# Kernel optimization log

Measured on AMD Instinct MI355X. Metric: run time of the kernel, lower is better.

## Reference

```python
import jax, jax.numpy as jnp
import numpy as np
from jax import lax

B, D, E, H, W = 256, 64, 16, 64, 64
PROJ, FC, NA = 512, 1024, 2

def _conv(x, w, pad):
    # x: [N,C,H,W], w: [O,I,kh,kw]
    return lax.conv_general_dilated(x, w, (1, 1), [(pad, pad), (pad, pad)],
                                    dimension_numbers=('NCHW', 'OIHW', 'NCHW'))

def _maxpool2(x):
    return lax.reduce_window(x, -jnp.inf, lax.max, (1, 1, 2, 2), (1, 1, 2, 2), 'VALID')

def _sample_conv(x, w, b):
    # per-sample conv with its own gathered expert weights: x [D,h,w], w [D,D,3,3]
    y = lax.conv_general_dilated(x[None], w, (1, 1), [(1, 1), (1, 1)],
                                 dimension_numbers=('NCHW', 'OIHW', 'NCHW'))[0]
    return y + b[:, None, None]

_expert_conv = jax.vmap(_sample_conv)  # batch of samples, each with its own kernel

def setup_inputs() -> dict:
    key = jax.random.key(0)
    ks = jax.random.split(key, 12)
    s = 0.05
    return {
        'image': jax.random.normal(ks[0], (B, 3, H, W), jnp.float32),
        'question': jax.random.randint(ks[1], (B, 8), 0, E),
        'stem_w0': jax.random.normal(ks[2], (D, 3, 3, 3), jnp.float32) * s,
        'stem_b0': jnp.zeros((D,), jnp.float32),
        'stem_w': jax.random.normal(ks[3], (3, D, D, 3, 3), jnp.float32) * s,
        'stem_b': jnp.zeros((3, D), jnp.float32),
        'exp_w1': jax.random.normal(ks[4], (E, D, D, 3, 3), jnp.float32) * s,
        'exp_b1': jnp.zeros((E, D), jnp.float32),
        'exp_w2': jax.random.normal(ks[5], (E, D, D, 3, 3), jnp.float32) * s,
        'exp_b2': jnp.zeros((E, D), jnp.float32),
        'proj_w': jax.random.normal(ks[6], (PROJ, D, 1, 1), jnp.float32) * s,
        'proj_b': jnp.zeros((PROJ,), jnp.float32),
        'fc1_w': jax.random.normal(ks[7], (FC, PROJ * 8 * 8), jnp.float32) * 0.01,
        'fc1_b': jnp.zeros((FC,), jnp.float32),
        'fc2_w': jax.random.normal(ks[8], (NA, FC), jnp.float32) * 0.01,
        'fc2_b': jnp.zeros((NA,), jnp.float32),
    }

def reference(image, question, stem_w0, stem_b0, stem_w, stem_b,
              exp_w1, exp_b1, exp_w2, exp_b2,
              proj_w, proj_b, fc1_w, fc1_b, fc2_w, fc2_b):
    # --- stem: 4 conv3x3 + ReLU, maxpool after layers 0 and 2 (64->32->16) ---
    h = jax.nn.relu(_conv(image, stem_w0, 1) + stem_b0[None, :, None, None])
    h = _maxpool2(h)
    h = jax.nn.relu(_conv(h, stem_w[0], 1) + stem_b[0][None, :, None, None])
    h = jax.nn.relu(_conv(h, stem_w[1], 1) + stem_b[1][None, :, None, None])
    h = _maxpool2(h)
    h = jax.nn.relu(_conv(h, stem_w[2], 1) + stem_b[2][None, :, None, None])
    # --- chain1 routing: cols (lhs=4, rel=5, rhs=7) each pick a ResidualBlock expert ---
    for col in (4, 5, 7):
        idx = question[:, col]                       # [B] expert ids
        w1, b1 = exp_w1[idx], exp_b1[idx]            # gather per-sample kernels
        w2, b2 = exp_w2[idx], exp_b2[idx]
        mid = jax.nn.relu(_expert_conv(h, w1, b1))   # conv1 + ReLU
        out = _expert_conv(mid, w2, b2)              # conv2 (no BN)
        h = jax.nn.relu(h + out)                     # residual + ReLU
    # --- classifier: 1x1 proj + ReLU, maxpool2, flatten, fc, fc ---
    c = jax.nn.relu(_conv(h, proj_w, 0) + proj_b[None, :, None, None])  # [B,512,16,16]
    c = _maxpool2(c)                                                     # [B,512,8,8]
    c = c.reshape(c.shape[0], -1)                                        # [B,32768]
    c = jax.nn.relu(c @ fc1_w.T + fc1_b)
    return c @ fc2_w.T + fc2_b                                           # [B,2]
```

## Files before the change

### kernel.cpp

```cpp
#include <hip/hip_runtime.h>
#include <cstddef>


typedef _Float16 half8 __attribute__((ext_vector_type(8)));
typedef _Float16 half4_t __attribute__((ext_vector_type(4)));
typedef float f32x4 __attribute__((ext_vector_type(4)));

#define LO_SCALE 2048.0f
#define LO_INV (1.0f / 2048.0f)

__global__ void transw_k(const float* __restrict__ src, float* __restrict__ dst,
                         int O, int I, int K, int total) {
    int id = blockIdx.x * 256 + threadIdx.x;
    if (id >= total) return;
    int OIK = O * I * K;
    int n = id / OIK, rem = id % OIK;
    int o = rem / (I * K), r2 = rem % (I * K);
    int i = r2 / K, k = r2 % K;
    dst[(size_t)n * OIK + (i * K + k) * O + o] = src[id];
}

__global__ void wxform_k(const float* __restrict__ src, _Float16* __restrict__ dst,
                         int nlayers) {
    int id = blockIdx.x * 256 + threadIdx.x;
    if (id >= nlayers * 36864) return;
    int layer = id / 36864, idx = id % 36864;
    int j = idx & 7, l = (idx >> 3) & 63, nt = (idx >> 9) & 3;
    int icc = (idx >> 11) & 1, tap = idx >> 12;
    int kl = (l >> 4) * 8 + j, ic = icc * 32 + kl, oc = nt * 16 + (l & 15);
    float v = src[(size_t)layer * 36864 + (oc * 64 + ic) * 9 + tap];
    _Float16 hi = (_Float16)v;
    _Float16 lo = (_Float16)((v - (float)hi) * LO_SCALE);
    dst[(size_t)layer * 73728 + idx] = hi;
    dst[(size_t)layer * 73728 + 36864 + idx] = lo;
}

__global__ void pwxform_k(const float* __restrict__ src, _Float16* __restrict__ dst) {
    int id = blockIdx.x * 256 + threadIdx.x;
    if (id >= 32768) return;
    int j = id & 7, l = (id >> 3) & 63, icc = (id >> 9) & 1, nt = id >> 10;
    int kl = (l >> 4) * 8 + j, ic = icc * 32 + kl, oc = nt * 16 + (l & 15);
    float v = src[oc * 64 + ic];
    _Float16 hi = (_Float16)v;
    _Float16 lo = (_Float16)((v - (float)hi) * LO_SCALE);
    dst[id] = hi;
    dst[32768 + id] = lo;
}

__global__ __launch_bounds__(256)
void conv1_k(const float* __restrict__ img, const float* __restrict__ w0t,
             const float* __restrict__ b0, float* __restrict__ out) {
    int b = blockIdx.x, tile = blockIdx.y, ocg = blockIdx.z;
    int typ = (tile >> 1) * 16, txp = (tile & 1) * 16;
    int cy0 = typ * 2, cx0 = txp * 2;
    __shared__ float lds[3][34][34];
    const float* imb = img + (size_t)b * 3 * 64 * 64;
    for (int i = threadIdx.x; i < 3 * 34 * 34; i += 256) {
        int c = i / 1156, rem = i % 1156, r = rem / 34, cc = rem % 34;
        int gy = cy0 - 1 + r, gx = cx0 - 1 + cc;
        float v = 0.f;
        if (gy >= 0 && gy < 64 && gx >= 0 && gx < 64) v = imb[(c * 64 + gy) * 64 + gx];
        lds[c][r][cc] = v;
    }
    __syncthreads();
    int pyl = threadIdx.x >> 4, pxl = threadIdx.x & 15;
    float win[3][4][4];
#pragma unroll
    for (int c = 0; c < 3; ++c)
#pragma unroll
        for (int wy = 0; wy < 4; ++wy)
#pragma unroll
            for (int wx = 0; wx < 4; ++wx)
                win[c][wy][wx] = lds[c][2 * pyl + wy][2 * pxl + wx];
    int py = typ + pyl, px = txp + pxl;
    float* op = &out[(((size_t)b * 32 + py) * 32 + px) * 64];
#pragma unroll
    for (int q = 0; q < 4; ++q) {
        int ocq = ocg * 4 + q;
        float acc[4][4] = {};
#pragma unroll
        for (int c = 0; c < 3; ++c)
#pragma unroll
            for (int ky = 0; ky < 3; ++ky)
#pragma unroll
                for (int kx = 0; kx < 3; ++kx) {
                    float4 w = *(const float4*)&w0t[(c * 9 + ky * 3 + kx) * 64 + ocq * 4];
                    float wv4[4] = {w.x, w.y, w.z, w.w};
#pragma unroll
                    for (int p2 = 0; p2 < 4; ++p2) {
                        float iv = win[c][(p2 >> 1) + ky][(p2 & 1) + kx];
#pragma unroll
                        for (int o = 0; o < 4; ++o)
                            acc[p2][o] = fmaf(iv, wv4[o], acc[p2][o]);
                    }
                }
        float4 res;
        float* rp = (float*)&res;
#pragma unroll
        for (int o = 0; o < 4; ++o) {
            float bvv = b0[ocq * 4 + o];
            float m = fmaxf(fmaxf(acc[0][o], acc[1][o]), fmaxf(acc[2][o], acc[3][o]));
            rp[o] = fmaxf(m + bvv, 0.f);
        }
        *(float4*)&op[ocq * 4] = res;
    }
}

template <int S, bool POOL, bool RES>
__global__ __launch_bounds__(256, 2)
void convm_k(const float* __restrict__ in, float* __restrict__ out,
             const _Float16* __restrict__ wf, const float* __restrict__ bias,
             const float* __restrict__ res, const int* __restrict__ question,
             int qcol) {
    int b = blockIdx.x, t = blockIdx.y;
    constexpr int NTX = S / 16;
    int ty0 = (t / NTX) * 8, tx0 = (t % NTX) * 16;

    __shared__ __align__(16) _Float16 lds[2 * 7200];

    int tid = threadIdx.x, lane = tid & 63, wv = tid >> 6;
    const _Float16* wb = wf;
    const float* bb = bias;
    if (question) {
        int idx = question[b * 8 + qcol];
        wb += (size_t)idx * 73728;
        bb += idx * 64;
    }
    float bv[4];
#pragma unroll
    for (int nt = 0; nt < 4; ++nt) bv[nt] = bb[nt * 16 + (lane & 15)];

    f32x4 acc1[2][4] = {};
    f32x4 acc2[2][4] = {};

    int am = lane & 15;
    int k0 = (lane >> 4) * 8;

    for (int icc = 0; icc < 2; ++icc) {
        __syncthreads();
        for (int i = tid; i < 1440; i += 256) {
            int pix = i >> 3, j4 = i & 7;
            int hy = pix / 18, hx = pix % 18;
            int gy = ty0 + hy - 1, gx = tx0 + hx - 1;
            float4 v = {0.f, 0.f, 0.f, 0.f};
            if (gy >= 0 && gy < S && gx >= 0 && gx < S)
                v = *(const float4*)&in[(((size_t)b * S + gy) * S + gx) * 64 + icc * 32 + j4 * 4];
            _Float16 h0 = (_Float16)v.x, h1 = (_Float16)v.y;
            _Float16 h2 = (_Float16)v.z, h3 = (_Float16)v.w;
            half4_t hh = {h0, h1, h2, h3};
            half4_t ll = {(_Float16)((v.x - (float)h0) * LO_SCALE),
                          (_Float16)((v.y - (float)h1) * LO_SCALE),
                          (_Float16)((v.z - (float)h2) * LO_SCALE),
                          (_Float16)((v.w - (float)h3) * LO_SCALE)};
            *(half4_t*)&lds[pix * 40 + j4 * 4] = hh;
            *(half4_t*)&lds[7200 + pix * 40 + j4 * 4] = ll;
        }
        __syncthreads();

#pragma unroll
        for (int ky = 0; ky < 3; ++ky)
#pragma unroll
            for (int kx = 0; kx < 3; ++kx) {
                int tap = ky * 3 + kx;
                const _Float16* wp = wb + (tap * 2 + icc) * 2048 + lane * 8;
                half8 bhi[4], blo[4];
#pragma unroll
                for (int nt = 0; nt < 4; ++nt) {
                    bhi[nt] = *(const half8*)(wp + nt * 512);
                    blo[nt] = *(const half8*)(wp + nt * 512 + 36864);
                }
#pragma unroll
                for (int mt = 0; mt < 2; ++mt) {
                    int MT = wv * 2 + mt;
                    int Q = MT * 4 + (am >> 2), s = am & 3;
                    int py = (Q >> 3) * 2 + (s >> 1), px = (Q & 7) * 2 + (s & 1);
                    const _Float16* ap = &lds[((py + ky) * 18 + (px + kx)) * 40 + k0];
                    half8 ahi = *(const half8*)ap;
                    half8 alo = *(const half8*)(ap + 7200);
#pragma unroll
                    for (int nt = 0; nt < 4; ++nt) {
                        acc1[mt][nt] = __builtin_amdgcn_mfma_f32_16x16x32_f16(
                            ahi, bhi[nt], acc1[mt][nt], 0, 0, 0);
                        acc2[mt][nt] = __builtin_amdgcn_mfma_f32_16x16x32_f16(
                            ahi, blo[nt], acc2[mt][nt], 0, 0, 0);
                        acc2[mt][nt] = __builtin_amdgcn_mfma_f32_16x16x32_f16(
                            alo, bhi[nt], acc2[mt][nt], 0, 0, 0);
                    }
                }
            }
    }

    int cn = lane & 15, rq = lane >> 4;
#pragma unroll
    for (int mt = 0; mt < 2; ++mt) {
        int MT = wv * 2 + mt;
        int Q = MT * 4 + rq;
        int qy = Q >> 3, qx = Q & 7;
#pragma unroll
        for (int nt = 0; nt < 4; ++nt) {
            int oc = nt * 16 + cn;
            float vals[4];
#pragma unroll
            for (int r = 0; r < 4; ++r)
                vals[r] = acc1[mt][nt][r] + acc2[mt][nt][r] * LO_INV + bv[nt];
            if (POOL) {
                float m = fmaxf(fmaxf(vals[0], vals[1]), fmaxf(vals[2], vals[3]));
                m = fmaxf(m, 0.f);
                int opy = (ty0 >> 1) + qy, opx = (tx0 >> 1) + qx;
                out[(((size_t)b * (S / 2) + opy) * (S / 2) + opx) * 64 + oc] = m;
            } else {
#pragma unroll
                for (int r = 0; r < 4; ++r) {
                    int py = qy * 2 + (r >> 1), px = qx * 2 + (r & 1);
                    size_t o = (((size_t)b * S + (ty0 + py)) * S + (tx0 + px)) * 64 + oc;
                    float v = vals[r];
                    if (RES) v += res[o];
                    out[o] = fmaxf(v, 0.f);
                }
            }
        }
    }
}

__global__ __launch_bounds__(256)
void projm_k(const float* __restrict__ in ,
             const _Float16* __restrict__ pw, const float* __restrict__ bias,
             _Float16* __restrict__ outh ) {
    int b = blockIdx.x;
    __shared__ float lt[64 * 65];
    int tid = threadIdx.x, lane = tid & 63, wv = tid >> 6;
    int row = lane & 15, cseg = lane >> 4;

    half8 ah[4][2], al[4][2];
#pragma unroll
    for (int mt = 0; mt < 4; ++mt) {
        int MT = wv * 4 + mt;
        int Q = MT * 4 + (row >> 2), s = row & 3;
        int y = (Q >> 3) * 2 + (s >> 1), x = (Q & 7) * 2 + (s & 1);
        const float* ip = in + ((size_t)b * 256 + y * 16 + x) * 64 + cseg * 8;
#pragma unroll
        for (int icc = 0; icc < 2; ++icc) {
            float4 v0 = *(const float4*)(ip + icc * 32);
            float4 v1 = *(const float4*)(ip + icc * 32 + 4);
            _Float16 h0 = (_Float16)v0.x, h1 = (_Float16)v0.y;
            _Float16 h2 = (_Float16)v0.z, h3 = (_Float16)v0.w;
            _Float16 h4 = (_Float16)v1.x, h5 = (_Float16)v1.y;
            _Float16 h6 = (_Float16)v1.z, h7 = (_Float16)v1.w;
            ah[mt][icc] = (half8){h0, h1, h2, h3, h4, h5, h6, h7};
            al[mt][icc] = (half8){(_Float16)((v0.x - (float)h0) * LO_SCALE),
                                  (_Float16)((v0.y - (float)h1) * LO_SCALE),
                                  (_Float16)((v0.z - (float)h2) * LO_SCALE),
                                  (_Float16)((v0.w - (float)h3) * LO_SCALE),
                                  (_Float16)((v1.x - (float)h4) * LO_SCALE),
                                  (_Float16)((v1.y - (float)h5) * LO_SCALE),
                                  (_Float16)((v1.z - (float)h6) * LO_SCALE),
                                  (_Float16)((v1.w - (float)h7) * LO_SCALE)};
        }
    }

    for (int ogl = 0; ogl < 4; ++ogl) {
        int og = blockIdx.y * 4 + ogl;
        half8 bh[4][2], bl[4][2];
#pragma unroll
        for (int ntl = 0; ntl < 4; ++ntl)
#pragma unroll
            for (int icc = 0; icc < 2; ++icc) {
                int nt = og * 4 + ntl;
                const _Float16* wp = pw + ((nt * 2 + icc) * 64 + lane) * 8;
                bh[ntl][icc] = *(const half8*)wp;
                bl[ntl][icc] = *(const half8*)(wp + 32768);
            }
        f32x4 a1[4][4] = {};
        f32x4 a2[4][4] = {};
#pragma unroll
        for (int icc = 0; icc < 2; ++icc)
#pragma unroll
            for (int mt = 0; mt < 4; ++mt)
#pragma unroll
                for (int ntl = 0; ntl < 4; ++ntl) {
                    a1[mt][ntl] = __builtin_amdgcn_mfma_f32_16x16x32_f16(
                        ah[mt][icc], bh[ntl][icc], a1[mt][ntl], 0, 0, 0);
                    a2[mt][ntl] = __builtin_amdgcn_mfma_f32_16x16x32_f16(
                        ah[mt][icc], bl[ntl][icc], a2[mt][ntl], 0, 0, 0);
                    a2[mt][ntl] = __builtin_amdgcn_mfma_f32_16x16x32_f16(
                        al[mt][icc], bh[ntl][icc], a2[mt][ntl], 0, 0, 0);
                }
        if (ogl) __syncthreads();
#pragma unroll
        for (int mt = 0; mt < 4; ++mt) {
            int Qg = (wv * 4 + mt) * 4 + (lane >> 4);
#pragma unroll
            for (int ntl = 0; ntl < 4; ++ntl) {
                float bvv = bias[og * 64 + ntl * 16 + (lane & 15)];
                float v0 = a1[mt][ntl][0] + a2[mt][ntl][0] * LO_INV + bvv;
                float v1 = a1[mt][ntl][1] + a2[mt][ntl][1] * LO_INV + bvv;
                float v2 = a1[mt][ntl][2] + a2[mt][ntl][2] * LO_INV + bvv;
                float v3 = a1[mt][ntl][3] + a2[mt][ntl][3] * LO_INV + bvv;
                float m = fmaxf(fmaxf(fmaxf(v0, v1), fmaxf(v2, v3)), 0.f);
                lt[(ntl * 16 + (lane & 15)) * 65 + Qg] = m;
            }
        }
        __syncthreads();
#pragma unroll
        for (int r = 0; r < 16; ++r) {
            int f = r * 256 + tid;
            int ol = f >> 6, q = f & 63;
            float v = lt[ol * 65 + q];
            _Float16 h = (_Float16)v;
            _Float16 l = (_Float16)((v - (float)h) * LO_SCALE);
            size_t o = (size_t)b * 32768 + og * 4096 + ol * 64 + q;
            outh[o] = h;
            outh[8388608 + o] = l;
        }
    }
}

__global__ __launch_bounds__(256)
void fc1m_k(const _Float16* __restrict__ Ahl ,
            const float* __restrict__ W,
            float* __restrict__ partial ) {
    int bid = blockIdx.x;
    int lid = (bid & 7) * 64 + (bid >> 3);
    int mt = lid & 1, nt = (lid >> 1) & 7, ks = lid >> 4;
    int m0 = mt * 128, n0 = nt * 128;
    const _Float16* Ab = Ahl + (size_t)m0 * 32768 + ks * 1024;
    const float* Wb = W + (size_t)n0 * 32768 + ks * 1024;

    __shared__ __align__(16) _Float16 lds[20480];
    _Float16* sa = lds;
    _Float16* sb = lds + 10240;

    int tid = threadIdx.x, lane = tid & 63, wv = tid >> 6;
    int wm = (wv & 1) * 64, wn = (wv >> 1) * 64;

    f32x4 acc1[4][4] = {};
    f32x4 acc2[4][4] = {};

    int arow[2], ak8[2];
#pragma unroll
    for (int p = 0; p < 2; ++p) {
        int idx = p * 256 + tid;
        arow[p] = idx >> 2;
        ak8[p] = (idx & 3) * 8;
    }
    int wrow[4], wc4[4];
#pragma unroll
    for (int p = 0; p < 4; ++p) {
        int idx = p * 256 + tid;
        wrow[p] = idx >> 3;
        wc4[p] = (idx & 7) << 2;
    }

    half8 pa_h[2], pa_l[2];
    float4 rw[4];
#pragma unroll
    for (int p = 0; p < 2; ++p) {
        pa_h[p] = *(const half8*)&Ab[(size_t)arow[p] * 32768 + ak8[p]];
        pa_l[p] = *(const half8*)&Ab[8388608 + (size_t)arow[p] * 32768 + ak8[p]];
    }
#pragma unroll
    for (int p = 0; p < 4; ++p)
        rw[p] = *(const float4*)&Wb[(size_t)wrow[p] * 32768 + wc4[p]];

    for (int kt = 0; kt < 32; ++kt) {
#pragma unroll
        for (int p = 0; p < 2; ++p) {
            *(half8*)&sa[arow[p] * 40 + ak8[p]] = pa_h[p];
            *(half8*)&sa[5120 + arow[p] * 40 + ak8[p]] = pa_l[p];
        }
#pragma unroll
        for (int p = 0; p < 4; ++p) {
            float4 u = rw[p];
            _Float16 g0 = (_Float16)u.x, g1 = (_Float16)u.y;
            _Float16 g2 = (_Float16)u.z, g3 = (_Float16)u.w;
            half4_t gh = {g0, g1, g2, g3};
            half4_t gl = {(_Float16)((u.x - (float)g0) * LO_SCALE),
                          (_Float16)((u.y - (float)g1) * LO_SCALE),
                          (_Float16)((u.z - (float)g2) * LO_SCALE),
                          (_Float16)((u.w - (float)g3) * LO_SCALE)};
            *(half4_t*)&sb[wrow[p] * 40 + wc4[p]] = gh;
            *(half4_t*)&sb[5120 + wrow[p] * 40 + wc4[p]] = gl;
        }
        __syncthreads();
        if (kt < 31) {
            int kb = (kt + 1) * 32;
#pragma unroll
            for (int p = 0; p < 2; ++p) {
                pa_h[p] = *(const half8*)&Ab[(size_t)arow[p] * 32768 + kb + ak8[p]];
                pa_l[p] = *(const half8*)&Ab[8388608 + (size_t)arow[p] * 32768 + kb + ak8[p]];
            }
#pragma unroll
            for (int p = 0; p < 4; ++p)
                rw[p] = *(const float4*)&Wb[(size_t)wrow[p] * 32768 + kb + wc4[p]];
        }
        int koff = (lane >> 4) * 8;
        int fr = lane & 15;
        half8 bh[4], bl[4];
#pragma unroll
        for (int nf = 0; nf < 4; ++nf) {
            int r = wn + nf * 16 + fr;
            bh[nf] = *(const half8*)&sb[r * 40 + koff];
            bl[nf] = *(const half8*)&sb[5120 + r * 40 + koff];
        }
#pragma unroll
        for (int mf = 0; mf < 4; ++mf) {
            int r = wm + mf * 16 + fr;
            half8 ah = *(const half8*)&sa[r * 40 + koff];
            half8 al = *(const half8*)&sa[5120 + r * 40 + koff];
#pragma unroll
            for (int nf = 0; nf < 4; ++nf) {
                acc1[mf][nf] = __builtin_amdgcn_mfma_f32_16x16x32_f16(
                    ah, bh[nf], acc1[mf][nf], 0, 0, 0);
                acc2[mf][nf] = __builtin_amdgcn_mfma_f32_16x16x32_f16(
                    ah, bl[nf], acc2[mf][nf], 0, 0, 0);
                acc2[mf][nf] = __builtin_amdgcn_mfma_f32_16x16x32_f16(
                    al, bh[nf], acc2[mf][nf], 0, 0, 0);
            }
        }
        __syncthreads();
    }

    int rq = lane >> 4, cn = lane & 15;
    float* pb = partial + (size_t)ks * 262144;
#pragma unroll
    for (int mf = 0; mf < 4; ++mf)
#pragma unroll
        for (int nf = 0; nf < 4; ++nf) {
            int n = n0 + wn + nf * 16 + cn;
#pragma unroll
            for (int r = 0; r < 4; ++r) {
                int m = m0 + wm + mf * 16 + rq * 4 + r;
                pb[(size_t)m * 1024 + n] = acc1[mf][nf][r] + acc2[mf][nf][r] * LO_INV;
            }
        }
}

__global__ __launch_bounds__(256)
void fc1red_k(const float* __restrict__ partial, const float* __restrict__ b1,
              float* __restrict__ fc1o_t ) {
    int m = blockIdx.x;
    int n0 = threadIdx.x * 4;
    float4 s = {0.f, 0.f, 0.f, 0.f};
    for (int ks = 0; ks < 32; ++ks) {
        float4 v = *(const float4*)&partial[((size_t)ks * 256 + m) * 1024 + n0];
        s.x += v.x; s.y += v.y; s.z += v.z; s.w += v.w;
    }
    fc1o_t[(size_t)(n0 + 0) * 256 + m] = fmaxf(s.x + b1[n0 + 0], 0.f);
    fc1o_t[(size_t)(n0 + 1) * 256 + m] = fmaxf(s.y + b1[n0 + 1], 0.f);
    fc1o_t[(size_t)(n0 + 2) * 256 + m] = fmaxf(s.z + b1[n0 + 2], 0.f);
    fc1o_t[(size_t)(n0 + 3) * 256 + m] = fmaxf(s.w + b1[n0 + 3], 0.f);
}

__global__ __launch_bounds__(256)
void fc2a_k(const float* __restrict__ a_t, const float* __restrict__ W2,
            float* __restrict__ p2) {
    int n2 = blockIdx.x, ks = blockIdx.y;
    int m = threadIdx.x;
    float acc = 0.f;
    for (int k = ks * 256; k < ks * 256 + 256; ++k)
        acc = fmaf(a_t[(size_t)k * 256 + m], W2[n2 * 1024 + k], acc);
    p2[((size_t)n2 * 4 + ks) * 256 + m] = acc;
}

__global__ __launch_bounds__(512)
void fc2b_k(const float* __restrict__ p2, const float* __restrict__ b2,
            float* __restrict__ out) {
    int i = threadIdx.x;
    int m = i >> 1, n2 = i & 1;
    float s = b2[n2];
#pragma unroll
    for (int ks = 0; ks < 4; ++ks) s += p2[((size_t)n2 * 4 + ks) * 256 + m];
    out[m * 2 + n2] = s;
}

extern "C" void kernel_launch(void* const* d_in, const int* in_sizes, int n_in,
                              void* d_out, int out_size, void* d_ws, size_t ws_size,
                              hipStream_t stream) {
    const float* image   = (const float*)d_in[0];
    const int*   question= (const int*)d_in[1];
    const float* stem_w0 = (const float*)d_in[2];
    const float* stem_b0 = (const float*)d_in[3];
    const float* stem_w  = (const float*)d_in[4];
    const float* stem_b  = (const float*)d_in[5];
    const float* exp_w1  = (const float*)d_in[6];
    const float* exp_b1  = (const float*)d_in[7];
    const float* exp_w2  = (const float*)d_in[8];
    const float* exp_b2  = (const float*)d_in[9];
    const float* proj_w  = (const float*)d_in[10];
    const float* proj_b  = (const float*)d_in[11];
    const float* fc1_w   = (const float*)d_in[12];
    const float* fc1_b   = (const float*)d_in[13];
    const float* fc2_w   = (const float*)d_in[14];
    const float* fc2_b   = (const float*)d_in[15];
    (void)in_sizes; (void)n_in; (void)out_size; (void)ws_size;

    float* ws = (float*)d_ws;
    const size_t A = 16777216, P2N = 4194304;
    float* p1    = ws;
    float* h2    = ws + A;
    float* p2    = ws + 2 * A;
    float* wtr   = ws + 2 * A + P2N;
    float* w0t   = wtr;
    _Float16* pwF = (_Float16*)(wtr + 1728);
    float* pfc2  = wtr + 1728 + 32768;
    _Float16* f16b = (_Float16*)(wtr + 36544);
    _Float16* stemtF = f16b;
    _Float16* e1tF   = f16b + 3 * 73728;
    _Float16* e2tF   = e1tF + 16 * 73728;
    float* hA    = ws;
    float* hB    = ws + P2N;
    float* hC    = ws + 2 * P2N;
    _Float16* pool3h = (_Float16*)h2;
    float* fc1o  = h2 + 8388608;
    float* fc1p  = ws;

    transw_k<<<(1728 + 255) / 256, 256, 0, stream>>>(stem_w0, w0t, 64, 3, 9, 1728);
    pwxform_k<<<128, 256, 0, stream>>>(proj_w, pwF);
    wxform_k<<<(3 * 36864 + 255) / 256, 256, 0, stream>>>(stem_w, stemtF, 3);
    wxform_k<<<(16 * 36864 + 255) / 256, 256, 0, stream>>>(exp_w1, e1tF, 16);
    wxform_k<<<(16 * 36864 + 255) / 256, 256, 0, stream>>>(exp_w2, e2tF, 16);

    conv1_k<<<dim3(256, 4, 4), 256, 0, stream>>>(image, w0t, stem_b0, p1);
    convm_k<32, false, false><<<dim3(256, 8), 256, 0, stream>>>(
        p1, h2, stemtF, stem_b, nullptr, nullptr, 0);
    convm_k<32, true, false><<<dim3(256, 8), 256, 0, stream>>>(
        h2, p2, stemtF + 73728, stem_b + 64, nullptr, nullptr, 0);
    convm_k<16, false, false><<<dim3(256, 2), 256, 0, stream>>>(
        p2, hA, stemtF + 2 * 73728, stem_b + 128, nullptr, nullptr, 0);

    const int cols[3] = {4, 5, 7};
    float* hin = hA;
    float* hmid = hB;
    float* hout = hC;
    for (int r = 0; r < 3; ++r) {
        convm_k<16, false, false><<<dim3(256, 2), 256, 0, stream>>>(
            hin, hmid, e1tF, exp_b1, nullptr, question, cols[r]);
        convm_k<16, false, true><<<dim3(256, 2), 256, 0, stream>>>(
            hmid, hout, e2tF, exp_b2, hin, question, cols[r]);
        float* tp = hin; hin = hout; hout = hmid; hmid = tp;
    }

    projm_k<<<dim3(256, 2), 256, 0, stream>>>(hin, pwF, proj_b, pool3h);
    fc1m_k<<<512, 256, 0, stream>>>(pool3h, fc1_w, fc1p);
    fc1red_k<<<256, 256, 0, stream>>>(fc1p, fc1_b, fc1o);
    fc2a_k<<<dim3(2, 4), 256, 0, stream>>>(fc1o, fc2_w, pfc2);
    fc2b_k<<<1, 512, 0, stream>>>(pfc2, fc2_b, (float*)d_out);
}
```

Measured before the change: 465.5 us.

## Double-buffer LDS tiles in fc1 GEMM to drop one barrier per k-step

The fc1 split-K GEMM now keeps two LDS buffers. Each iteration writes the next k-tile (including the fp32-to-fp16 hi/lo split of W) into the alternate buffer while MFMAs read the current one, and prefetches global data two tiles ahead. This removes the second barrier per iteration and lets the LDS writes overlap compute, at the cost of doubling LDS to 80 KB per block, which may reduce occupancy. It also adds a min-blocks hint to conv1's launch bounds.

```diff
diff --git a/kernel.cpp b/kernel.cpp
--- a/kernel.cpp
+++ b/kernel.cpp
@@ -47,7 +47,7 @@
     dst[32768 + id] = lo;
 }
 
-__global__ __launch_bounds__(256)
+__global__ __launch_bounds__(256, 4)
 void conv1_k(const float* __restrict__ img, const float* __restrict__ w0t,
              const float* __restrict__ b0, float* __restrict__ out) {
     int b = blockIdx.x, tile = blockIdx.y, ocg = blockIdx.z;
@@ -326,12 +326,11 @@
     const _Float16* Ab = Ahl + (size_t)m0 * 32768 + ks * 1024;
     const float* Wb = W + (size_t)n0 * 32768 + ks * 1024;
 
-    __shared__ __align__(16) _Float16 lds[20480];
-    _Float16* sa = lds;
-    _Float16* sb = lds + 10240;
+    __shared__ __align__(16) _Float16 lds[40960];
 
     int tid = threadIdx.x, lane = tid & 63, wv = tid >> 6;
     int wm = (wv & 1) * 64, wn = (wv >> 1) * 64;
+    int koff = (lane >> 4) * 8, fr = lane & 15;
 
     f32x4 acc1[4][4] = {};
     f32x4 acc2[4][4] = {};
@@ -353,6 +352,7 @@
 
     half8 pa_h[2], pa_l[2];
     float4 rw[4];
+
 #pragma unroll
     for (int p = 0; p < 2; ++p) {
         pa_h[p] = *(const half8*)&Ab[(size_t)arow[p] * 32768 + ak8[p]];
@@ -361,12 +361,12 @@
 #pragma unroll
     for (int p = 0; p < 4; ++p)
         rw[p] = *(const float4*)&Wb[(size_t)wrow[p] * 32768 + wc4[p]];
-
-    for (int kt = 0; kt < 32; ++kt) {
+    {
+        _Float16* b0p = lds;
 #pragma unroll
         for (int p = 0; p < 2; ++p) {
-            *(half8*)&sa[arow[p] * 40 + ak8[p]] = pa_h[p];
-            *(half8*)&sa[5120 + arow[p] * 40 + ak8[p]] = pa_l[p];
+            *(half8*)&b0p[arow[p] * 40 + ak8[p]] = pa_h[p];
+            *(half8*)&b0p[5120 + arow[p] * 40 + ak8[p]] = pa_l[p];
         }
 #pragma unroll
         for (int p = 0; p < 4; ++p) {
@@ -378,35 +378,66 @@
                           (_Float16)((u.y - (float)g1) * LO_SCALE),
                           (_Float16)((u.z - (float)g2) * LO_SCALE),
                           (_Float16)((u.w - (float)g3) * LO_SCALE)};
-            *(half4_t*)&sb[wrow[p] * 40 + wc4[p]] = gh;
-            *(half4_t*)&sb[5120 + wrow[p] * 40 + wc4[p]] = gl;
-        }
-        __syncthreads();
+            *(half4_t*)&b0p[10240 + wrow[p] * 40 + wc4[p]] = gh;
+            *(half4_t*)&b0p[15360 + wrow[p] * 40 + wc4[p]] = gl;
+        }
+    }
+#pragma unroll
+    for (int p = 0; p < 2; ++p) {
+        pa_h[p] = *(const half8*)&Ab[(size_t)arow[p] * 32768 + 32 + ak8[p]];
+        pa_l[p] = *(const half8*)&Ab[8388608 + (size_t)arow[p] * 32768 + 32 + ak8[p]];
+    }
+#pragma unroll
+    for (int p = 0; p < 4; ++p)
+        rw[p] = *(const float4*)&Wb[(size_t)wrow[p] * 32768 + 32 + wc4[p]];
+    __syncthreads();
+
+    for (int kt = 0; kt < 32; ++kt) {
+        _Float16* cur = lds + (kt & 1) * 20480;
+        _Float16* nxt = lds + ((kt + 1) & 1) * 20480;
         if (kt < 31) {
-            int kb = (kt + 1) * 32;
 #pragma unroll
             for (int p = 0; p < 2; ++p) {
-                pa_h[p] = *(const half8*)&Ab[(size_t)arow[p] * 32768 + kb + ak8[p]];
-                pa_l[p] = *(const half8*)&Ab[8388608 + (size_t)arow[p] * 32768 + kb + ak8[p]];
-            }
-#pragma unroll
-            for (int p = 0; p < 4; ++p)
-                rw[p] = *(const float4*)&Wb[(size_t)wrow[p] * 32768 + kb + wc4[p]];
-        }
-        int koff = (lane >> 4) * 8;
-        int fr = lane & 15;
+                *(half8*)&nxt[arow[p] * 40 + ak8[p]] = pa_h[p];
+                *(half8*)&nxt[5120 + arow[p] * 40 + ak8[p]] = pa_l[p];
+            }
+#pragma unroll
+            for (int p = 0; p < 4; ++p) {
+                float4 u = rw[p];
+                _Float16 g0 = (_Float16)u.x, g1 = (_Float16)u.y;
+                _Float16 g2 = (_Float16)u.z, g3 = (_Float16)u.w;
+                half4_t gh = {g0, g1, g2, g3};
+                half4_t gl = {(_Float16)((u.x - (float)g0) * LO_SCALE),
+                              (_Float16)((u.y - (float)g1) * LO_SCALE),
+                              (_Float16)((u.z - (float)g2) * LO_SCALE),
+                              (_Float16)((u.w - (float)g3) * LO_SCALE)};
+                *(half4_t*)&nxt[10240 + wrow[p] * 40 + wc4[p]] = gh;
+                *(half4_t*)&nxt[15360 + wrow[p] * 40 + wc4[p]] = gl;
+            }
+            if (kt < 30) {
+                int kb = (kt + 2) * 32;
+#pragma unroll
+                for (int p = 0; p < 2; ++p) {
+                    pa_h[p] = *(const half8*)&Ab[(size_t)arow[p] * 32768 + kb + ak8[p]];
+                    pa_l[p] = *(const half8*)&Ab[8388608 + (size_t)arow[p] * 32768 + kb + ak8[p]];
+                }
+#pragma unroll
+                for (int p = 0; p < 4; ++p)
+                    rw[p] = *(const float4*)&Wb[(size_t)wrow[p] * 32768 + kb + wc4[p]];
+            }
+        }
         half8 bh[4], bl[4];
 #pragma unroll
         for (int nf = 0; nf < 4; ++nf) {
             int r = wn + nf * 16 + fr;
-            bh[nf] = *(const half8*)&sb[r * 40 + koff];
-            bl[nf] = *(const half8*)&sb[5120 + r * 40 + koff];
+            bh[nf] = *(const half8*)&cur[10240 + r * 40 + koff];
+            bl[nf] = *(const half8*)&cur[15360 + r * 40 + koff];
         }
 #pragma unroll
         for (int mf = 0; mf < 4; ++mf) {
             int r = wm + mf * 16 + fr;
-            half8 ah = *(const half8*)&sa[r * 40 + koff];
-            half8 al = *(const half8*)&sa[5120 + r * 40 + koff];
+            half8 ah = *(const half8*)&cur[r * 40 + koff];
+            half8 al = *(const half8*)&cur[5120 + r * 40 + koff];
 #pragma unroll
             for (int nf = 0; nf < 4; ++nf) {
                 acc1[mf][nf] = __builtin_amdgcn_mfma_f32_16x16x32_f16(
```

After: 468.4 us. Within noise of the previous version (+0.6%).
